# Kernel tuning notes

Measured on AMD Instinct MI355X. Metric: run time of the kernel, lower is better.

## Reference

```python
import jax, jax.numpy as jnp
import numpy as np

N_NODES = 50000
E_DIR = 250000
IN_FEATS = 256
N_HIDDEN = 64
N_CLASSES = 40
HEADS = 4
NEG_SLOPE = 0.2


def _build_graph():
    # mirrors to_undirected(edge_index) then add_self_loops(...)
    rng = np.random.default_rng(0)
    s = rng.integers(0, N_NODES, E_DIR)
    d = rng.integers(0, N_NODES, E_DIR)
    edges = np.stack([np.concatenate([s, d]), np.concatenate([d, s])], axis=0)
    edges = np.unique(edges, axis=1)  # dedup, as to_undirected does
    loops = np.arange(N_NODES)
    src = np.concatenate([edges[0], loops]).astype(np.int32)
    dst = np.concatenate([edges[1], loops]).astype(np.int32)
    return jnp.asarray(src), jnp.asarray(dst)


def setup_inputs() -> dict:
    key = jax.random.key(0)
    ks = jax.random.split(key, 16)
    src, dst = _build_graph()
    x = jax.random.uniform(ks[0], (N_NODES, IN_FEATS), dtype=jnp.float32)
    scale = 0.05
    # layer 0: IN -> HEADS*N_HIDDEN
    W0 = jax.random.normal(ks[1], (IN_FEATS, HEADS * N_HIDDEN), dtype=jnp.float32) * scale
    al0 = jax.random.normal(ks[2], (HEADS, N_HIDDEN), dtype=jnp.float32) * scale
    ar0 = jax.random.normal(ks[3], (HEADS, N_HIDDEN), dtype=jnp.float32) * scale
    b0 = jnp.zeros((HEADS * N_HIDDEN,), dtype=jnp.float32)
    # layer 1: HEADS*N_HIDDEN -> HEADS*N_HIDDEN
    W1 = jax.random.normal(ks[4], (HEADS * N_HIDDEN, HEADS * N_HIDDEN), dtype=jnp.float32) * scale
    al1 = jax.random.normal(ks[5], (HEADS, N_HIDDEN), dtype=jnp.float32) * scale
    ar1 = jax.random.normal(ks[6], (HEADS, N_HIDDEN), dtype=jnp.float32) * scale
    b1 = jnp.zeros((HEADS * N_HIDDEN,), dtype=jnp.float32)
    # layer 2: HEADS*N_HIDDEN -> HEADS*N_CLASSES (mean over heads at the end)
    W2 = jax.random.normal(ks[7], (HEADS * N_HIDDEN, HEADS * N_CLASSES), dtype=jnp.float32) * scale
    al2 = jax.random.normal(ks[8], (HEADS, N_CLASSES), dtype=jnp.float32) * scale
    ar2 = jax.random.normal(ks[9], (HEADS, N_CLASSES), dtype=jnp.float32) * scale
    b2 = jnp.zeros((HEADS * N_CLASSES,), dtype=jnp.float32)
    return {"x": x, "src": src, "dst": dst,
            "W0": W0, "al0": al0, "ar0": ar0, "b0": b0,
            "W1": W1, "al1": al1, "ar1": ar1, "b1": b1,
            "W2": W2, "al2": al2, "ar2": ar2, "b2": b2}


def _gat_layer(h, W, al, ar, b, src, dst):
    # DGL GATConv (no dropout, no residual): fc -> per-head attention -> edge softmax -> scatter-sum
    n = h.shape[0]
    nh, f = al.shape
    feat = (h @ W).reshape(n, nh, f)                      # [N,H,F]
    el = jnp.einsum('nhf,hf->nh', feat, al)               # [N,H]
    er = jnp.einsum('nhf,hf->nh', feat, ar)               # [N,H]
    e = jax.nn.leaky_relu(el[src] + er[dst], NEG_SLOPE)   # [E,H]
    emax = jax.lax.stop_gradient(jax.ops.segment_max(e, dst, num_segments=n))
    ee = jnp.exp(e - emax[dst])
    denom = jax.ops.segment_sum(ee, dst, num_segments=n)  # [N,H], >0 (self-loops)
    alpha = ee / denom[dst]                               # edge softmax over incoming edges
    msg = feat[src] * alpha[:, :, None]                   # [E,H,F]
    out = jax.ops.segment_sum(msg, dst, num_segments=n)   # [N,H,F]
    return out + b.reshape(1, nh, f)


def reference(x, src, dst, W0, al0, ar0, b0, W1, al1, ar1, b1, W2, al2, ar2, b2):
    n = x.shape[0]
    # x.shape[1] != 8189 -> row-normalize with clamp(min=1)
    h = x / jnp.clip(jnp.sum(x, axis=1, keepdims=True), 1.0)
    h = jax.nn.elu(_gat_layer(h, W0, al0, ar0, b0, src, dst)).reshape(n, -1)
    h = jax.nn.elu(_gat_layer(h, W1, al1, ar1, b1, src, dst)).reshape(n, -1)
    logits = _gat_layer(h, W2, al2, ar2, b2, src, dst).mean(axis=1)  # mean over heads
    return jax.nn.log_softmax(logits, axis=1)
```

## Files before the change

kernel.cpp:

```cpp
#include <hip/hip_runtime.h>
#include <math.h>

#define HEADS 4
#define HID 64
#define NCLS 40
#define IN_FEATS 256
#define NEG_SLOPE 0.2f
#define CAP 64
#define FP8_S 256.0f

typedef __attribute__((ext_vector_type(8))) short short8;
typedef __attribute__((ext_vector_type(4))) float floatx4;
typedef __attribute__((ext_vector_type(2))) float floatx2;

__device__ __forceinline__ ushort f2bf(float x) {
    union { float f; unsigned u; } v; v.f = x;
    unsigned r = (v.u + 0x7fff + ((v.u >> 16) & 1)) >> 16;
    return (ushort)r;
}
__device__ __forceinline__ unsigned char f2fp8(float x) {
    int pk = __builtin_amdgcn_cvt_pk_fp8_f32(x, x, 0, false);
    return (unsigned char)(pk & 0xff);
}

__global__ __launch_bounds__(256) void k_prep(const int* __restrict__ src,
                                              int* __restrict__ rowptr, int Em, int rb,
                                              const float* __restrict__ W0,
                                              const float* __restrict__ W1,
                                              const float* __restrict__ W2,
                                              ushort* __restrict__ Wt0,
                                              ushort* __restrict__ Wt1,
                                              ushort* __restrict__ Wt2,
                                              const float* __restrict__ x,
                                              ushort* __restrict__ A16, int n) {
    int b = blockIdx.x;
    if (b < rb) {
        int j = b * 256 + threadIdx.x;
        if (j <= Em) {
            if (j == 0) {
                int hi = src[0];
                for (int v = 0; v <= hi; ++v) rowptr[v] = 0;
            } else if (j == Em) {
                int lo = src[Em - 1];
                for (int v = lo + 1; v <= n; ++v) rowptr[v] = Em;
            } else {
                int a = src[j - 1], c = src[j];
                for (int v = a + 1; v <= c; ++v) rowptr[v] = j;
            }
        }
        return;
    }
    b -= rb;
    if (b < 256) {
        int idx = b * 256 + threadIdx.x;
        int k = idx >> 8, c = idx & 255;
        Wt0[c * 256 + k] = f2bf(W0[idx]);
        Wt1[c * 256 + k] = f2bf(W1[idx]);
        if (idx < 40960) {
            int k2 = idx / 160, c2 = idx - k2 * 160;
            Wt2[c2 * 256 + k2] = f2bf(W2[idx]);
        }
        return;
    }
    b -= 256;
    int row = b * 4 + (threadIdx.x >> 6);
    if (row >= n) return;
    int lane = threadIdx.x & 63;
    float4 v = reinterpret_cast<const float4*>(x + (size_t)row * 256)[lane];
    float s = v.x + v.y + v.z + v.w;
    for (int off = 32; off; off >>= 1) s += __shfl_down(s, off);
    s = __shfl(s, 0);
    float inv = 1.0f / fmaxf(s, 1.0f);
    ushort4 o;
    o.x = f2bf(v.x * inv); o.y = f2bf(v.y * inv);
    o.z = f2bf(v.z * inv); o.w = f2bf(v.w * inv);
    reinterpret_cast<ushort4*>(A16 + (size_t)row * 256)[lane] = o;
}

#define LDP 72

__global__ __launch_bounds__(256) void k_gemm_mfma(const ushort* __restrict__ A16,
                                                   const ushort* __restrict__ Wt,
                                                   unsigned char* __restrict__ Out8,
                                                   int n, int NCOL) {
    __shared__ ushort As[128 * LDP];
    __shared__ ushort Bs[128 * LDP];
    int t = threadIdx.x;
    int lane = t & 63;
    int w = t >> 6;
    int wrow = (w & 1) * 64;
    int wcol = (w >> 1) * 64;
    int row0 = blockIdx.x * 128;
    int col0 = blockIdx.y * 128;
    int lrow = lane & 15;
    int kq = lane >> 4;

    floatx4 acc[4][4];
#pragma unroll
    for (int i = 0; i < 4; ++i)
#pragma unroll
        for (int j = 0; j < 4; ++j) acc[i][j] = (floatx4)(0.f);

    for (int k0 = 0; k0 < 256; k0 += 64) {
#pragma unroll
        for (int p = 0; p < 4; ++p) {
            int idx = p * 256 + t;
            int r = idx >> 3;
            int kk = (idx & 7) * 8;
            int gr = row0 + r; gr = (gr < n) ? gr : (n - 1);
            uint4 v = *reinterpret_cast<const uint4*>(&A16[(size_t)gr * 256 + k0 + kk]);
            *reinterpret_cast<uint4*>(&As[r * LDP + kk]) = v;
        }
#pragma unroll
        for (int p = 0; p < 4; ++p) {
            int idx = p * 256 + t;
            int c = idx >> 3;
            int kk = (idx & 7) * 8;
            int gc = col0 + c; gc = (gc < NCOL) ? gc : (NCOL - 1);
            uint4 v = *reinterpret_cast<const uint4*>(&Wt[(size_t)gc * 256 + k0 + kk]);
            *reinterpret_cast<uint4*>(&Bs[c * LDP + kk]) = v;
        }
        __syncthreads();

#pragma unroll
        for (int kc = 0; kc < 2; ++kc) {
            int kb = kc * 32 + kq * 8;
            short8 af[4], bf[4];
#pragma unroll
            for (int i = 0; i < 4; ++i)
                af[i] = *reinterpret_cast<const short8*>(&As[(wrow + 16 * i + lrow) * LDP + kb]);
#pragma unroll
            for (int j = 0; j < 4; ++j)
                bf[j] = *reinterpret_cast<const short8*>(&Bs[(wcol + 16 * j + lrow) * LDP + kb]);
#pragma unroll
            for (int i = 0; i < 4; ++i)
#pragma unroll
                for (int j = 0; j < 4; ++j)
                    acc[i][j] = __builtin_amdgcn_mfma_f32_16x16x32_bf16(af[i], bf[j], acc[i][j], 0, 0, 0);
        }
        __syncthreads();
    }

#pragma unroll
    for (int j = 0; j < 4; ++j) {
        int c = col0 + wcol + 16 * j + lrow;
        if (c >= NCOL) continue;
#pragma unroll
        for (int i = 0; i < 4; ++i) {
            int rbase = row0 + wrow + 16 * i + kq * 4;
#pragma unroll
            for (int r = 0; r < 4; ++r) {
                int gr = rbase + r;
                if (gr < n) Out8[(size_t)gr * NCOL + c] = f2fp8(acc[i][j][r] * FP8_S);
            }
        }
    }
}

__global__ __launch_bounds__(256) void k_elr2(const unsigned char* __restrict__ F8,
                                              const float* __restrict__ al,
                                              const float* __restrict__ ar,
                                              float* __restrict__ el,
                                              float* __restrict__ er, int n, int Fh) {
    __shared__ float sbuf[256], rbuf[256];
    int t = threadIdx.x;
    int node = blockIdx.x * 4 + (t >> 6);
    int lane = t & 63;
    int RL = 4 * Fh;
    bool act = (4 * lane < RL) && (node < n);
    float sl = 0.f, sr = 0.f;
    if (act) {
        unsigned u = *reinterpret_cast<const unsigned*>(&F8[(size_t)node * RL + 4 * lane]);
        floatx2 p01 = __builtin_amdgcn_cvt_pk_f32_fp8(u, false);
        floatx2 p23 = __builtin_amdgcn_cvt_pk_f32_fp8(u, true);
        float4 av = *reinterpret_cast<const float4*>(&al[4 * lane]);
        float4 bv = *reinterpret_cast<const float4*>(&ar[4 * lane]);
        sl = p01.x * av.x + p01.y * av.y + p23.x * av.z + p23.y * av.w;
        sr = p01.x * bv.x + p01.y * bv.y + p23.x * bv.z + p23.y * bv.w;
    }
    sbuf[t] = sl; rbuf[t] = sr;
    __syncthreads();
    int seg = Fh >> 2;
    if (lane < 4 && node < n) {
        int b = (t & ~63) + lane * seg;
        float asum = 0.f, bsum = 0.f;
        for (int q = 0; q < seg; ++q) { asum += sbuf[b + q]; bsum += rbuf[b + q]; }
        el[node * 4 + lane] = asum * (1.0f / FP8_S);
        er[node * 4 + lane] = bsum * (1.0f / FP8_S);
    }
}

template <int Fh, bool FINAL>
__global__ __launch_bounds__(256) void k_agg9(const unsigned char* __restrict__ F8,
                                              const float* __restrict__ el,
                                              const float* __restrict__ er,
                                              const int* __restrict__ rowptr,
                                              const int* __restrict__ dstv,
                                              const float* __restrict__ bias,
                                              ushort* __restrict__ out16,
                                              float* __restrict__ outF,
                                              int n) {
    constexpr int RL = 4 * Fh;
    constexpr bool FULL = (RL == 256);
    __shared__ float wls[4][CAP * 4];
    __shared__ int   mls[4][CAP];
    __shared__ float fbuf[4][FINAL ? 160 : 1];
    int wid = threadIdx.x >> 6;
    int node = blockIdx.x * 4 + wid;
    if (node >= n) node = n - 1;
    int lane = threadIdx.x & 63;
    int lo = rowptr[node];
    int deg_main = rowptr[node + 1] - lo;
    if (deg_main > CAP - 1) deg_main = CAP - 1;
    int deg = deg_main + 1;

    float* wl = wls[wid];
    int*   ml = mls[wid];

    int h = lane & 3;
    float ern = er[node * 4 + h];
    float wr[4];
    float s = 0.f;
    int ecount = 0;
    for (int e = lane >> 2; e < deg; e += 16) {
        int mid = (e < deg_main) ? dstv[lo + e] : node;
        if (h == 0) ml[e] = mid;
        float x = el[mid * 4 + h] + ern;
        x = (x > 0.f) ? x : NEG_SLOPE * x;
        float w = __expf(x);
        wr[ecount++] = w;
        s += w;
    }
#pragma unroll
    for (int off = 4; off < 64; off <<= 1) s += __shfl_xor(s, off);
    float invd = (1.0f / FP8_S) / s;
    {
        int e = lane >> 2;
        for (int i = 0; i < ecount; ++i, e += 16) wl[e * 4 + h] = wr[i] * invd;
    }
    __syncthreads();

    int my = 4 * lane;
    bool act = FULL || (my < RL);
    int hB = FULL ? (lane >> 4) : (my / Fh);
    float a0 = 0.f, a1 = 0.f, a2 = 0.f, a3 = 0.f;
#pragma unroll 4
    for (int j = 0; j < deg; ++j) {
        int mid = ml[j];
        float w = wl[j * 4 + hB];
        unsigned u = 0u;
        if (act) u = *reinterpret_cast<const unsigned*>(&F8[(size_t)mid * RL + my]);
        floatx2 p01 = __builtin_amdgcn_cvt_pk_f32_fp8(u, false);
        floatx2 p23 = __builtin_amdgcn_cvt_pk_f32_fp8(u, true);
        a0 = fmaf(w, p01.x, a0);
        a1 = fmaf(w, p01.y, a1);
        a2 = fmaf(w, p23.x, a2);
        a3 = fmaf(w, p23.y, a3);
    }

    if (!FINAL) {
        if (act) {
            float4 b4 = *reinterpret_cast<const float4*>(&bias[my]);
            float o0 = a0 + b4.x, o1 = a1 + b4.y, o2 = a2 + b4.z, o3 = a3 + b4.w;
            o0 = (o0 > 0.f) ? o0 : (__expf(o0) - 1.0f);
            o1 = (o1 > 0.f) ? o1 : (__expf(o1) - 1.0f);
            o2 = (o2 > 0.f) ? o2 : (__expf(o2) - 1.0f);
            o3 = (o3 > 0.f) ? o3 : (__expf(o3) - 1.0f);
            uint2 pk;
            pk.x = (unsigned)f2bf(o0) | ((unsigned)f2bf(o1) << 16);
            pk.y = (unsigned)f2bf(o2) | ((unsigned)f2bf(o3) << 16);
            *reinterpret_cast<uint2*>(&out16[(size_t)node * RL + my]) = pk;
        }
    } else {
        if (act) {
            float4 b4 = *reinterpret_cast<const float4*>(&bias[my]);
            fbuf[wid][my + 0] = a0 + b4.x;
            fbuf[wid][my + 1] = a1 + b4.y;
            fbuf[wid][my + 2] = a2 + b4.z;
            fbuf[wid][my + 3] = a3 + b4.w;
        }
        __syncthreads();
        float val = 0.f;
        if (lane < 40)
            val = 0.25f * (fbuf[wid][lane] + fbuf[wid][40 + lane] +
                           fbuf[wid][80 + lane] + fbuf[wid][120 + lane]);
        float mx = (lane < 40) ? val : -1e30f;
#pragma unroll
        for (int off = 32; off; off >>= 1) mx = fmaxf(mx, __shfl_xor(mx, off));
        float ex = (lane < 40) ? __expf(val - mx) : 0.f;
        float se = ex;
#pragma unroll
        for (int off = 32; off; off >>= 1) se += __shfl_xor(se, off);
        if (lane < 40) outF[(size_t)node * 40 + lane] = val - mx - logf(se);
    }
}

extern "C" void kernel_launch(void* const* d_in, const int* in_sizes, int n_in,
                              void* d_out, int out_size, void* d_ws, size_t ws_size,
                              hipStream_t stream) {
    const float* x  = (const float*)d_in[0];
    const int* src  = (const int*)d_in[1];
    const int* dst  = (const int*)d_in[2];
    const float* W0 = (const float*)d_in[3];
    const float* al0 = (const float*)d_in[4];
    const float* ar0 = (const float*)d_in[5];
    const float* b0 = (const float*)d_in[6];
    const float* W1 = (const float*)d_in[7];
    const float* al1 = (const float*)d_in[8];
    const float* ar1 = (const float*)d_in[9];
    const float* b1 = (const float*)d_in[10];
    const float* W2 = (const float*)d_in[11];
    const float* al2 = (const float*)d_in[12];
    const float* ar2 = (const float*)d_in[13];
    const float* b2 = (const float*)d_in[14];
    float* out = (float*)d_out;

    const int n = in_sizes[0] / IN_FEATS;
    const int E = in_sizes[1];
    const int Em = E - n;

    char* base = (char*)d_ws;
    size_t off = 0;
    auto alloc = [&](size_t bytes) {
        void* p = base + off;
        off = (off + bytes + 255) & ~(size_t)255;
        return p;
    };
    ushort* A16 = (ushort*)alloc((size_t)n * 256 * 2);
    unsigned char* F8 = (unsigned char*)alloc((size_t)n * 256);
    ushort* Wt0 = (ushort*)alloc((size_t)256 * 256 * 2);
    ushort* Wt1 = (ushort*)alloc((size_t)256 * 256 * 2);
    ushort* Wt2 = (ushort*)alloc((size_t)160 * 256 * 2);
    float* el  = (float*)alloc((size_t)n * HEADS * 4);
    float* er  = (float*)alloc((size_t)n * HEADS * 4);
    int* rowptr = (int*)alloc((size_t)(n + 1) * 4);
    (void)ws_size; (void)n_in; (void)out_size;

    const int rb = (Em + 1 + 255) / 256;
    const int nb4 = (n + 3) / 4;
    const int gemm_rows = (n + 127) / 128;

    k_prep<<<rb + 256 + nb4, 256, 0, stream>>>(src, rowptr, Em, rb,
                                               W0, W1, W2, Wt0, Wt1, Wt2, x, A16, n);

    k_gemm_mfma<<<dim3(gemm_rows, 2), 256, 0, stream>>>(A16, Wt0, F8, n, 256);
    k_elr2<<<nb4, 256, 0, stream>>>(F8, al0, ar0, el, er, n, HID);
    k_agg9<HID, false><<<nb4, 256, 0, stream>>>(F8, el, er, rowptr, dst, b0, A16, out, n);

    k_gemm_mfma<<<dim3(gemm_rows, 2), 256, 0, stream>>>(A16, Wt1, F8, n, 256);
    k_elr2<<<nb4, 256, 0, stream>>>(F8, al1, ar1, el, er, n, HID);
    k_agg9<HID, false><<<nb4, 256, 0, stream>>>(F8, el, er, rowptr, dst, b1, A16, out, n);

    k_gemm_mfma<<<dim3(gemm_rows, 2), 256, 0, stream>>>(A16, Wt2, F8, n, 160);
    k_elr2<<<nb4, 256, 0, stream>>>(F8, al2, ar2, el, er, n, NCLS);
    k_agg9<NCLS, true><<<nb4, 256, 0, stream>>>(F8, el, er, rowptr, dst, b2, nullptr, out, n);
}
```

Baseline: 319.1 us.

## Fuse attention-logit projections into GEMM via precomputed W·a matrices

```diff
diff --git a/kernel.cpp b/kernel.cpp
--- a/kernel.cpp
+++ b/kernel.cpp
@@ -31,6 +31,11 @@
                                               ushort* __restrict__ Wt0,
                                               ushort* __restrict__ Wt1,
                                               ushort* __restrict__ Wt2,
+                                              const float* __restrict__ al0,
+                                              const float* __restrict__ ar0,
+                                              const float* __restrict__ al1,
+                                              const float* __restrict__ ar1,
+                                              ushort* __restrict__ Wel,
                                               const float* __restrict__ x,
                                               ushort* __restrict__ A16, int n) {
     int b = blockIdx.x;
@@ -63,6 +68,27 @@
         return;
     }
     b -= 256;
+    if (b < 64) {
+        int idx = b * 256 + threadIdx.x;
+        int l = idx >> 13;
+        int rem = idx & 8191;
+        int y = rem >> 12;
+        int rem2 = rem & 4095;
+        int r = rem2 >> 8;
+        int k = rem2 & 255;
+        float sum = 0.f;
+        if (r < 4) {
+            const float* W = l ? W1 : W0;
+            const float* av = (r < 2) ? (l ? al1 : al0) : (l ? ar1 : ar0);
+            int h = 2 * y + (r & 1);
+            const float* wrow = W + (size_t)k * 256 + h * 64;
+            const float* arow = av + h * 64;
+            for (int f = 0; f < 64; ++f) sum += wrow[f] * arow[f];
+        }
+        Wel[idx] = f2bf(sum);
+        return;
+    }
+    b -= 64;
     int row = b * 4 + (threadIdx.x >> 6);
     if (row >= n) return;
     int lane = threadIdx.x & 63;
@@ -78,13 +104,19 @@
 }
 
 #define LDP 72
-
+#define LDW 264
+
+template <bool FUSE_EL>
 __global__ __launch_bounds__(256) void k_gemm_mfma(const ushort* __restrict__ A16,
                                                    const ushort* __restrict__ Wt,
+                                                   const ushort* __restrict__ Welg,
                                                    unsigned char* __restrict__ Out8,
+                                                   float* __restrict__ elv,
+                                                   float* __restrict__ erv,
                                                    int n, int NCOL) {
     __shared__ ushort As[128 * LDP];
     __shared__ ushort Bs[128 * LDP];
+    __shared__ ushort Wls[FUSE_EL ? 16 * LDW : 1];
     int t = threadIdx.x;
     int lane = t & 63;
     int w = t >> 6;
@@ -95,11 +127,26 @@
     int lrow = lane & 15;
     int kq = lane >> 4;
 
+    if (FUSE_EL) {
+        const ushort* wg = Welg + blockIdx.y * 4096;
+#pragma unroll
+        for (int p = 0; p < 2; ++p) {
+            int idx = p * 256 + t;
+            int r = idx >> 5;
+            int kk = (idx & 31) * 8;
+            uint4 v = *reinterpret_cast<const uint4*>(&wg[r * 256 + kk]);
+            *reinterpret_cast<uint4*>(&Wls[r * LDW + kk]) = v;
+        }
+    }
+
     floatx4 acc[4][4];
-#pragma unroll
-    for (int i = 0; i < 4; ++i)
+    floatx4 acc_e[4];
+#pragma unroll
+    for (int i = 0; i < 4; ++i) {
+        acc_e[i] = (floatx4)(0.f);
 #pragma unroll
         for (int j = 0; j < 4; ++j) acc[i][j] = (floatx4)(0.f);
+    }
 
     for (int k0 = 0; k0 < 256; k0 += 64) {
 #pragma unroll
@@ -137,6 +184,12 @@
 #pragma unroll
                 for (int j = 0; j < 4; ++j)
                     acc[i][j] = __builtin_amdgcn_mfma_f32_16x16x32_bf16(af[i], bf[j], acc[i][j], 0, 0, 0);
+            if (FUSE_EL && wcol == 0) {
+                short8 bw = *reinterpret_cast<const short8*>(&Wls[lrow * LDW + kb]);
+#pragma unroll
+                for (int i = 0; i < 4; ++i)
+                    acc_e[i] = __builtin_amdgcn_mfma_f32_16x16x32_bf16(af[i], bw, acc_e[i], 0, 0, 0);
+            }
         }
         __syncthreads();
     }
@@ -152,6 +205,22 @@
             for (int r = 0; r < 4; ++r) {
                 int gr = rbase + r;
                 if (gr < n) Out8[(size_t)gr * NCOL + c] = f2fp8(acc[i][j][r] * FP8_S);
+            }
+        }
+    }
+    if (FUSE_EL && wcol == 0 && lrow < 4) {
+        int y2 = blockIdx.y * 2;
+#pragma unroll
+        for (int i = 0; i < 4; ++i) {
+            int rbase = row0 + wrow + 16 * i + kq * 4;
+#pragma unroll
+            for (int r = 0; r < 4; ++r) {
+                int gr = rbase + r;
+                if (gr < n) {
+                    float v = acc_e[i][r];
+                    if (lrow < 2) elv[gr * 4 + y2 + lrow] = v;
+                    else          erv[gr * 4 + y2 + (lrow - 2)] = v;
+                }
             }
         }
     }
@@ -331,6 +400,7 @@
     ushort* Wt0 = (ushort*)alloc((size_t)256 * 256 * 2);
     ushort* Wt1 = (ushort*)alloc((size_t)256 * 256 * 2);
     ushort* Wt2 = (ushort*)alloc((size_t)160 * 256 * 2);
+    ushort* Wel = (ushort*)alloc((size_t)16384 * 2);
     float* el  = (float*)alloc((size_t)n * HEADS * 4);
     float* er  = (float*)alloc((size_t)n * HEADS * 4);
     int* rowptr = (int*)alloc((size_t)(n + 1) * 4);
@@ -340,18 +410,17 @@
     const int nb4 = (n + 3) / 4;
     const int gemm_rows = (n + 127) / 128;
 
-    k_prep<<<rb + 256 + nb4, 256, 0, stream>>>(src, rowptr, Em, rb,
-                                               W0, W1, W2, Wt0, Wt1, Wt2, x, A16, n);
-
-    k_gemm_mfma<<<dim3(gemm_rows, 2), 256, 0, stream>>>(A16, Wt0, F8, n, 256);
-    k_elr2<<<nb4, 256, 0, stream>>>(F8, al0, ar0, el, er, n, HID);
+    k_prep<<<rb + 256 + 64 + nb4, 256, 0, stream>>>(src, rowptr, Em, rb,
+                                                    W0, W1, W2, Wt0, Wt1, Wt2,
+                                                    al0, ar0, al1, ar1, Wel, x, A16, n);
+
+    k_gemm_mfma<true><<<dim3(gemm_rows, 2), 256, 0, stream>>>(A16, Wt0, Wel, F8, el, er, n, 256);
     k_agg9<HID, false><<<nb4, 256, 0, stream>>>(F8, el, er, rowptr, dst, b0, A16, out, n);
 
-    k_gemm_mfma<<<dim3(gemm_rows, 2), 256, 0, stream>>>(A16, Wt1, F8, n, 256);
-    k_elr2<<<nb4, 256, 0, stream>>>(F8, al1, ar1, el, er, n, HID);
+    k_gemm_mfma<true><<<dim3(gemm_rows, 2), 256, 0, stream>>>(A16, Wt1, Wel + 8192, F8, el, er, n, 256);
     k_agg9<HID, false><<<nb4, 256, 0, stream>>>(F8, el, er, rowptr, dst, b1, A16, out, n);
 
-    k_gemm_mfma<<<dim3(gemm_rows, 2), 256, 0, stream>>>(A16, Wt2, F8, n, 160);
+    k_gemm_mfma<false><<<dim3(gemm_rows, 2), 256, 0, stream>>>(A16, Wt2, nullptr, F8, nullptr, nullptr, n, 160);
     k_elr2<<<nb4, 256, 0, stream>>>(F8, al2, ar2, el, er, n, NCLS);
     k_agg9<NCLS, true><<<nb4, 256, 0, stream>>>(F8, el, er, rowptr, dst, b2, nullptr, out, n);
 }
```

Result: faster. 292.7 us (-8.3%).
